# Kernel tuning notes

Hardware: AMD Instinct MI355X
Metric: run time of the kernel (lower is better)

## Reference

```python
import jax, jax.numpy as jnp
import numpy as np

HEAD_SIZE = 128
BLOCK_SIZE = 2048


def setup_inputs() -> dict:
    key = jax.random.key(0)
    kx, kk, kq, kv = jax.random.split(key, 4)
    B, T, C = 8, 2048, HEAD_SIZE
    s = 1.0 / np.sqrt(C)
    x = jax.random.normal(kx, (B, T, C), dtype=jnp.float32)
    Wk = jax.random.normal(kk, (C, C), dtype=jnp.float32) * s
    Wq = jax.random.normal(kq, (C, C), dtype=jnp.float32) * s
    Wv = jax.random.normal(kv, (C, C), dtype=jnp.float32) * s
    return {"x": x, "Wk": Wk, "Wq": Wq, "Wv": Wv}


def reference(x, Wk, Wq, Wv):
    B, T, C = x.shape
    # nn.Linear(C, C, bias=False): y = x @ W.T
    k = jnp.einsum('btc,dc->btd', x, Wk)
    q = jnp.einsum('btc,dc->btd', x, Wq)
    v = jnp.einsum('btc,dc->btd', x, Wv)
    scores = jnp.einsum('btd,bsd->bts', q, k) * (C ** -0.5)  # [B,T,T]
    causal = jnp.tril(jnp.ones((T, T), dtype=bool))
    scores = jnp.where(causal, scores, -jnp.inf)
    weights = jax.nn.softmax(scores, axis=-1)
    return jnp.einsum('bts,bsd->btd', weights, v)
```

## Files before the change

kernel.cpp:

```cpp
#include <hip/hip_runtime.h>

#define T_SEQ 2048
#define C_DIM 128
#define S_QK 0.08838834764831845f

typedef __attribute__((ext_vector_type(8))) short bf16x8;
typedef __attribute__((ext_vector_type(4))) float f32x4;

#define OPART_OFF 12582912UL
#define ML_OFF    31457280UL
#define XBF_OFF   31752192UL
#define WBF_OFF   35946496UL

__device__ __forceinline__ unsigned short f2bf(float f) {
    union { float f; unsigned int u; } v; v.f = f;
    unsigned int r = v.u + 0x7FFFu + ((v.u >> 16) & 1u);
    return (unsigned short)(r >> 16);
}

__device__ __forceinline__ int chunk_base(int qt) {
    int g = qt >> 3;
    if (g == 1) return (qt - 8) * 2;
    if (g == 2) return 16 + (qt - 16) * 3;
    return 40 + (qt - 24) * 4;
}

__global__ __launch_bounds__(256) void prep_kernel(
    const float* __restrict__ x,
    const float* __restrict__ Wk, const float* __restrict__ Wq,
    const float* __restrict__ Wv,
    unsigned short* __restrict__ xbf, unsigned short* __restrict__ wbf)
{
    int idx = blockIdx.x * 256 + threadIdx.x;
    const float* src;
    unsigned short* dst;
    float scale = 1.0f;
    if (idx < 524288) {
        src = x + (size_t)idx * 4;
        dst = xbf + (size_t)idx * 4;
    } else {
        int wi  = idx - 524288;
        int sel = wi >> 12;
        int off = (wi & 4095) * 4;
        src = (sel == 0 ? Wq : sel == 1 ? Wk : Wv) + off;
        dst = wbf + sel * 16384 + off;
        if (sel == 0) scale = S_QK;
    }
    float4 v = *reinterpret_cast<const float4*>(src);
    ushort4 o;
    o.x = f2bf(v.x * scale); o.y = f2bf(v.y * scale);
    o.z = f2bf(v.z * scale); o.w = f2bf(v.w * scale);
    *reinterpret_cast<ushort4*>(dst) = o;
}

__global__ __launch_bounds__(256) void proj_kernel(
    const unsigned short* __restrict__ xbf,
    const unsigned short* __restrict__ wbf,
    unsigned short* __restrict__ qo, unsigned short* __restrict__ ko,
    unsigned short* __restrict__ vto)
{
    const int rt = blockIdx.x;
    const int z  = blockIdx.y;
    const int tid  = threadIdx.x;
    const int lane = tid & 63;
    const int w    = tid >> 6;
    const int n16  = lane & 15;
    const int quad = lane >> 4;

    __shared__ __align__(16) unsigned short Wl[128 * 136];
    __shared__ __align__(16) unsigned short Xl[9216];

    const unsigned short* Wsrc = wbf + z * 16384;
    #pragma unroll
    for (int i = 0; i < 8; ++i) {
        int e = (tid + i * 256) * 8;
        int r = e >> 7, c = e & 127;
        *reinterpret_cast<uint4*>(&Wl[r * 136 + c]) =
            *reinterpret_cast<const uint4*>(Wsrc + e);
    }
    const unsigned short* xrow = xbf + (size_t)rt * 64 * C_DIM;
    #pragma unroll
    for (int i = 0; i < 4; ++i) {
        int e = (tid + i * 256) * 8;
        int r = e >> 7, c = e & 127;
        *reinterpret_cast<uint4*>(&Xl[r * 136 + c]) =
            *reinterpret_cast<const uint4*>(xrow + e);
    }
    __syncthreads();

    const int arow = w * 16 + n16;
    bf16x8 afr[4];
    #pragma unroll
    for (int kk = 0; kk < 4; ++kk)
        afr[kk] = *reinterpret_cast<const bf16x8*>(&Xl[arow * 136 + kk * 32 + quad * 8]);

    f32x4 acc[8];
    #pragma unroll
    for (int nt = 0; nt < 8; ++nt) acc[nt] = (f32x4){0.f, 0.f, 0.f, 0.f};
    #pragma unroll
    for (int kk = 0; kk < 4; ++kk)
        #pragma unroll
        for (int nt = 0; nt < 8; ++nt) {
            bf16x8 bfr = *reinterpret_cast<const bf16x8*>(
                &Wl[(nt * 16 + n16) * 136 + kk * 32 + quad * 8]);
            acc[nt] = __builtin_amdgcn_mfma_f32_16x16x32_bf16(afr[kk], bfr, acc[nt], 0, 0, 0);
        }

    const int trow_base = w * 16 + quad * 4;
    __syncthreads();
    if (z < 2) {
        #pragma unroll
        for (int nt = 0; nt < 8; ++nt)
            #pragma unroll
            for (int r = 0; r < 4; ++r)
                Xl[(trow_base + r) * 136 + nt * 16 + n16] = f2bf(acc[nt][r]);
        __syncthreads();
        unsigned short* dst = (z == 0 ? qo : ko) + (size_t)rt * 64 * C_DIM;
        #pragma unroll
        for (int i = 0; i < 4; ++i) {
            int e = (tid + i * 256) * 8;
            int r = e >> 7, c = e & 127;
            *reinterpret_cast<uint4*>(dst + e) =
                *reinterpret_cast<const uint4*>(&Xl[r * 136 + c]);
        }
    } else {
        const int b  = rt >> 5;
        const int qt = rt & 31;
        #pragma unroll
        for (int nt = 0; nt < 8; ++nt)
            #pragma unroll
            for (int r = 0; r < 4; ++r)
                Xl[(nt * 16 + n16) * 72 + trow_base + r] = f2bf(acc[nt][r]);
        __syncthreads();
        unsigned short* dst = vto + (size_t)b * C_DIM * T_SEQ + (size_t)qt * 64;
        #pragma unroll
        for (int i = 0; i < 4; ++i) {
            int e = tid + i * 256;
            int d = e >> 3, cv = (e & 7) * 8;
            *reinterpret_cast<uint4*>(dst + (size_t)d * T_SEQ + cv) =
                *reinterpret_cast<const uint4*>(&Xl[d * 72 + cv]);
        }
    }
}

__global__ __launch_bounds__(256) void attn_kernel(
    const unsigned short* __restrict__ qb,
    const unsigned short* __restrict__ kb,
    const unsigned short* __restrict__ vtb,
    float* __restrict__ opart, float2* __restrict__ mlbuf,
    float* __restrict__ out)
{
    const int qt    = blockIdx.x;
    const int chunk = blockIdx.y;
    const int b     = blockIdx.z;
    if (chunk * 8 > qt) return;

    const int tid  = threadIdx.x;
    const int lane = tid & 63;
    const int w    = tid >> 6;
    const int n16  = lane & 15;
    const int quad = lane >> 4;

    __shared__ __align__(16) unsigned short Kl[64 * 136];
    __shared__ __align__(16) unsigned short Vl[128 * 72];
    __shared__ __align__(16) unsigned short Pl[4][16 * 72];

    const size_t bT = (size_t)b * T_SEQ;
    const int qbase = qt * 64 + w * 16;

    bf16x8 qfr[4];
    #pragma unroll
    for (int kk = 0; kk < 4; ++kk)
        qfr[kk] = *reinterpret_cast<const bf16x8*>(
            qb + (bT + qbase + n16) * C_DIM + kk * 32 + quad * 8);

    f32x4 o[8];
    #pragma unroll
    for (int ct = 0; ct < 8; ++ct) o[ct] = (f32x4){0.f, 0.f, 0.f, 0.f};
    float m[4], l[4];
    #pragma unroll
    for (int r = 0; r < 4; ++r) { m[r] = -INFINITY; l[r] = 0.f; }

    const int k0 = chunk * 8;
    const int k1 = min(k0 + 8, qt + 1);

    for (int kt = k0; kt < k1; ++kt) {
        __syncthreads();
        const unsigned short* ks = kb + (bT + (size_t)kt * 64) * C_DIM;
        #pragma unroll
        for (int i = 0; i < 4; ++i) {
            int e = tid + i * 256;
            int r = e >> 4, c = (e & 15) * 8;
            *reinterpret_cast<uint4*>(&Kl[r * 136 + c]) =
                *reinterpret_cast<const uint4*>(ks + r * 128 + c);
        }
        const unsigned short* vs = vtb + (size_t)b * C_DIM * T_SEQ + (size_t)kt * 64;
        #pragma unroll
        for (int i = 0; i < 4; ++i) {
            int e = tid + i * 256;
            int d = e >> 3, c = (e & 7) * 8;
            *reinterpret_cast<uint4*>(&Vl[d * 72 + c]) =
                *reinterpret_cast<const uint4*>(vs + (size_t)d * T_SEQ + c);
        }
        __syncthreads();

        f32x4 s[4];
        #pragma unroll
        for (int nt = 0; nt < 4; ++nt) s[nt] = (f32x4){0.f, 0.f, 0.f, 0.f};
        #pragma unroll
        for (int kk = 0; kk < 4; ++kk)
            #pragma unroll
            for (int nt = 0; nt < 4; ++nt) {
                bf16x8 bfr = *reinterpret_cast<const bf16x8*>(
                    &Kl[(nt * 16 + n16) * 136 + kk * 32 + quad * 8]);
                s[nt] = __builtin_amdgcn_mfma_f32_16x16x32_bf16(qfr[kk], bfr, s[nt], 0, 0, 0);
            }

        if (kt == qt) {
            #pragma unroll
            for (int nt = 0; nt < 4; ++nt)
                #pragma unroll
                for (int r = 0; r < 4; ++r) {
                    int sabs = kt * 64 + nt * 16 + n16;
                    int qabs = qbase + quad * 4 + r;
                    if (sabs > qabs) s[nt][r] = -1e30f;
                }
        }

        float alpha[4];
        #pragma unroll
        for (int r = 0; r < 4; ++r) {
            float tmax = fmaxf(fmaxf(s[0][r], s[1][r]), fmaxf(s[2][r], s[3][r]));
            #pragma unroll
            for (int off = 1; off < 16; off <<= 1)
                tmax = fmaxf(tmax, __shfl_xor(tmax, off));
            float mn = fmaxf(m[r], tmax);
            alpha[r] = __expf(m[r] - mn);
            float tsum = 0.f;
            #pragma unroll
            for (int nt = 0; nt < 4; ++nt) {
                float p = __expf(s[nt][r] - mn);
                s[nt][r] = p;
                tsum += p;
            }
            #pragma unroll
            for (int off = 1; off < 16; off <<= 1)
                tsum += __shfl_xor(tsum, off);
            l[r] = l[r] * alpha[r] + tsum;
            m[r] = mn;
        }
        #pragma unroll
        for (int ct = 0; ct < 8; ++ct)
            #pragma unroll
            for (int r = 0; r < 4; ++r)
                o[ct][r] *= alpha[r];

        unsigned short* pw = Pl[w];
        #pragma unroll
        for (int nt = 0; nt < 4; ++nt)
            #pragma unroll
            for (int r = 0; r < 4; ++r)
                pw[(quad * 4 + r) * 72 + nt * 16 + n16] = f2bf(s[nt][r]);

        #pragma unroll
        for (int kk2 = 0; kk2 < 2; ++kk2) {
            bf16x8 afr = *reinterpret_cast<const bf16x8*>(
                &pw[n16 * 72 + kk2 * 32 + quad * 8]);
            #pragma unroll
            for (int ct = 0; ct < 8; ++ct) {
                bf16x8 bfr = *reinterpret_cast<const bf16x8*>(
                    &Vl[(ct * 16 + n16) * 72 + kk2 * 32 + quad * 8]);
                o[ct] = __builtin_amdgcn_mfma_f32_16x16x32_bf16(afr, bfr, o[ct], 0, 0, 0);
            }
        }
    }

    if (qt < 8) {
        float* outp = out + (bT + qbase) * C_DIM;
        #pragma unroll
        for (int r = 0; r < 4; ++r) {
            float inv = 1.0f / l[r];
            #pragma unroll
            for (int ct = 0; ct < 8; ++ct)
                outp[(size_t)(quad * 4 + r) * C_DIM + ct * 16 + n16] = o[ct][r] * inv;
        }
    } else {
        const int slot = b * 72 + chunk_base(qt) + chunk;
        float* op = opart + (size_t)slot * 8192;
        #pragma unroll
        for (int r = 0; r < 4; ++r) {
            int row = w * 16 + quad * 4 + r;
            #pragma unroll
            for (int ct = 0; ct < 8; ++ct)
                op[row * 128 + ct * 16 + n16] = o[ct][r];
            if (n16 == 0)
                mlbuf[(size_t)slot * 64 + row] = make_float2(m[r], l[r]);
        }
    }
}

__global__ __launch_bounds__(256) void merge_kernel(
    const float* __restrict__ opart, const float2* __restrict__ mlbuf,
    float* __restrict__ out)
{
    const int qt = 8 + blockIdx.x;
    const int b  = blockIdx.y;
    const int nch  = (qt >> 3) + 1;
    const int base = b * 72 + chunk_base(qt);
    const int row = threadIdx.x >> 2;
    const int c0  = (threadIdx.x & 3) * 32;

    float mi[4], li[4], wgt[4];
    float M = -INFINITY;
    for (int i = 0; i < nch; ++i) {
        float2 t = mlbuf[(size_t)(base + i) * 64 + row];
        mi[i] = t.x; li[i] = t.y;
        M = fmaxf(M, t.x);
    }
    float L = 0.f;
    for (int i = 0; i < nch; ++i) {
        wgt[i] = __expf(mi[i] - M);
        L += li[i] * wgt[i];
    }
    const float inv = 1.0f / L;

    float* orow = out + ((size_t)(b * T_SEQ + qt * 64 + row)) * C_DIM;
    #pragma unroll
    for (int j = 0; j < 8; ++j) {
        int col = c0 + j * 4;
        float ax = 0.f, ay = 0.f, az = 0.f, aw = 0.f;
        for (int i = 0; i < nch; ++i) {
            float4 p = *reinterpret_cast<const float4*>(
                opart + (size_t)(base + i) * 8192 + row * 128 + col);
            ax += wgt[i] * p.x; ay += wgt[i] * p.y;
            az += wgt[i] * p.z; aw += wgt[i] * p.w;
        }
        float4 r4; r4.x = ax * inv; r4.y = ay * inv; r4.z = az * inv; r4.w = aw * inv;
        *reinterpret_cast<float4*>(orow + col) = r4;
    }
}

extern "C" void kernel_launch(void* const* d_in, const int* in_sizes, int n_in,
                              void* d_out, int out_size, void* d_ws, size_t ws_size,
                              hipStream_t stream) {
    const float* x  = (const float*)d_in[0];
    const float* Wk = (const float*)d_in[1];
    const float* Wq = (const float*)d_in[2];
    const float* Wv = (const float*)d_in[3];

    unsigned short* qw  = (unsigned short*)d_ws;
    unsigned short* kw  = qw + 2097152;
    unsigned short* vw  = kw + 2097152;
    float*          opart = (float*)((char*)d_ws + OPART_OFF);
    float2*         mlb   = (float2*)((char*)d_ws + ML_OFF);
    unsigned short* xbf   = (unsigned short*)((char*)d_ws + XBF_OFF);
    unsigned short* wbf   = (unsigned short*)((char*)d_ws + WBF_OFF);

    prep_kernel<<<2096, 256, 0, stream>>>(x, Wk, Wq, Wv, xbf, wbf);
    proj_kernel<<<dim3(256, 3), 256, 0, stream>>>(xbf, wbf, qw, kw, vw);
    attn_kernel<<<dim3(32, 4, 8), 256, 0, stream>>>(qw, kw, vw, opart, mlb, (float*)d_out);
    merge_kernel<<<dim3(24, 8), 256, 0, stream>>>(opart, mlb, (float*)d_out);
}
```

Baseline: 135.7 us.

## Fuse bf16 conversion into projection, split KV finer, prefetch tiles, bf16 partials

Drops the separate prep kernel: the projection kernel now reads fp32 x and weights directly and converts them to bf16 while staging into shared memory. Attention KV chunks shrink from 8 to 4 tiles, which doubles the split-K grid to improve load balance, and the merge kernel now handles up to 8 partials. The next K/V tiles are prefetched into registers during compute. Partial outputs are stored as bf16 to halve merge traffic. The costs are extra partial slots, higher register pressure, and a small precision loss in the partials.

```diff
diff --git a/kernel.cpp b/kernel.cpp
--- a/kernel.cpp
+++ b/kernel.cpp
@@ -7,55 +7,27 @@
 typedef __attribute__((ext_vector_type(8))) short bf16x8;
 typedef __attribute__((ext_vector_type(4))) float f32x4;
 
-#define OPART_OFF 12582912UL
-#define ML_OFF    31457280UL
-#define XBF_OFF   31752192UL
-#define WBF_OFF   35946496UL
+#define ML_OFF 30932992UL
 
 __device__ __forceinline__ unsigned short f2bf(float f) {
     union { float f; unsigned int u; } v; v.f = f;
     unsigned int r = v.u + 0x7FFFu + ((v.u >> 16) & 1u);
     return (unsigned short)(r >> 16);
 }
-
-__device__ __forceinline__ int chunk_base(int qt) {
-    int g = qt >> 3;
-    if (g == 1) return (qt - 8) * 2;
-    if (g == 2) return 16 + (qt - 16) * 3;
-    return 40 + (qt - 24) * 4;
-}
-
-__global__ __launch_bounds__(256) void prep_kernel(
+__device__ __forceinline__ float bf2f(unsigned short s) {
+    union { unsigned int u; float f; } v; v.u = ((unsigned int)s) << 16;
+    return v.f;
+}
+
+__device__ __forceinline__ int chunk_base4(int qt) {
+    int g = qt >> 2;
+    return 2 * (g - 1) * (g + 2) + (qt - 4 * g) * (g + 1);
+}
+
+__global__ __launch_bounds__(256) void proj_kernel(
     const float* __restrict__ x,
-    const float* __restrict__ Wk, const float* __restrict__ Wq,
+    const float* __restrict__ Wq, const float* __restrict__ Wk,
     const float* __restrict__ Wv,
-    unsigned short* __restrict__ xbf, unsigned short* __restrict__ wbf)
-{
-    int idx = blockIdx.x * 256 + threadIdx.x;
-    const float* src;
-    unsigned short* dst;
-    float scale = 1.0f;
-    if (idx < 524288) {
-        src = x + (size_t)idx * 4;
-        dst = xbf + (size_t)idx * 4;
-    } else {
-        int wi  = idx - 524288;
-        int sel = wi >> 12;
-        int off = (wi & 4095) * 4;
-        src = (sel == 0 ? Wq : sel == 1 ? Wk : Wv) + off;
-        dst = wbf + sel * 16384 + off;
-        if (sel == 0) scale = S_QK;
-    }
-    float4 v = *reinterpret_cast<const float4*>(src);
-    ushort4 o;
-    o.x = f2bf(v.x * scale); o.y = f2bf(v.y * scale);
-    o.z = f2bf(v.z * scale); o.w = f2bf(v.w * scale);
-    *reinterpret_cast<ushort4*>(dst) = o;
-}
-
-__global__ __launch_bounds__(256) void proj_kernel(
-    const unsigned short* __restrict__ xbf,
-    const unsigned short* __restrict__ wbf,
     unsigned short* __restrict__ qo, unsigned short* __restrict__ ko,
     unsigned short* __restrict__ vto)
 {
@@ -70,21 +42,28 @@
     __shared__ __align__(16) unsigned short Wl[128 * 136];
     __shared__ __align__(16) unsigned short Xl[9216];
 
-    const unsigned short* Wsrc = wbf + z * 16384;
+    const float* W = (z == 0) ? Wq : (z == 1) ? Wk : Wv;
+    const float scale = (z == 0) ? S_QK : 1.0f;
+
+    #pragma unroll
+    for (int i = 0; i < 16; ++i) {
+        int e = (tid + i * 256) * 4;
+        int r = e >> 7, c = e & 127;
+        float4 v = *reinterpret_cast<const float4*>(W + e);
+        ushort4 o4;
+        o4.x = f2bf(v.x * scale); o4.y = f2bf(v.y * scale);
+        o4.z = f2bf(v.z * scale); o4.w = f2bf(v.w * scale);
+        *reinterpret_cast<ushort4*>(&Wl[r * 136 + c]) = o4;
+    }
+    const float* xr = x + (size_t)rt * 64 * C_DIM;
     #pragma unroll
     for (int i = 0; i < 8; ++i) {
-        int e = (tid + i * 256) * 8;
+        int e = (tid + i * 256) * 4;
         int r = e >> 7, c = e & 127;
-        *reinterpret_cast<uint4*>(&Wl[r * 136 + c]) =
-            *reinterpret_cast<const uint4*>(Wsrc + e);
-    }
-    const unsigned short* xrow = xbf + (size_t)rt * 64 * C_DIM;
-    #pragma unroll
-    for (int i = 0; i < 4; ++i) {
-        int e = (tid + i * 256) * 8;
-        int r = e >> 7, c = e & 127;
-        *reinterpret_cast<uint4*>(&Xl[r * 136 + c]) =
-            *reinterpret_cast<const uint4*>(xrow + e);
+        float4 v = *reinterpret_cast<const float4*>(xr + e);
+        ushort4 o4;
+        o4.x = f2bf(v.x); o4.y = f2bf(v.y); o4.z = f2bf(v.z); o4.w = f2bf(v.w);
+        *reinterpret_cast<ushort4*>(&Xl[r * 136 + c]) = o4;
     }
     __syncthreads();
 
@@ -147,13 +126,13 @@
     const unsigned short* __restrict__ qb,
     const unsigned short* __restrict__ kb,
     const unsigned short* __restrict__ vtb,
-    float* __restrict__ opart, float2* __restrict__ mlbuf,
+    unsigned short* __restrict__ opart, float2* __restrict__ mlbuf,
     float* __restrict__ out)
 {
     const int qt    = blockIdx.x;
     const int chunk = blockIdx.y;
     const int b     = blockIdx.z;
-    if (chunk * 8 > qt) return;
+    if (chunk * 4 > qt) return;
 
     const int tid  = threadIdx.x;
     const int lane = tid & 63;
@@ -181,28 +160,53 @@
     #pragma unroll
     for (int r = 0; r < 4; ++r) { m[r] = -INFINITY; l[r] = 0.f; }
 
-    const int k0 = chunk * 8;
-    const int k1 = min(k0 + 8, qt + 1);
+    const int k0 = chunk * 4;
+    const int k1 = min(k0 + 4, qt + 1);
+
+    uint4 kreg[4], vreg[4];
+    {
+        const unsigned short* ks = kb + (bT + (size_t)k0 * 64) * C_DIM;
+        #pragma unroll
+        for (int i = 0; i < 4; ++i) {
+            int e = tid + i * 256;
+            kreg[i] = *reinterpret_cast<const uint4*>(ks + (e >> 4) * 128 + (e & 15) * 8);
+        }
+        const unsigned short* vs = vtb + (size_t)b * C_DIM * T_SEQ + (size_t)k0 * 64;
+        #pragma unroll
+        for (int i = 0; i < 4; ++i) {
+            int e = tid + i * 256;
+            vreg[i] = *reinterpret_cast<const uint4*>(vs + (size_t)(e >> 3) * T_SEQ + (e & 7) * 8);
+        }
+    }
 
     for (int kt = k0; kt < k1; ++kt) {
         __syncthreads();
-        const unsigned short* ks = kb + (bT + (size_t)kt * 64) * C_DIM;
-        #pragma unroll
-        for (int i = 0; i < 4; ++i) {
-            int e = tid + i * 256;
-            int r = e >> 4, c = (e & 15) * 8;
-            *reinterpret_cast<uint4*>(&Kl[r * 136 + c]) =
-                *reinterpret_cast<const uint4*>(ks + r * 128 + c);
-        }
-        const unsigned short* vs = vtb + (size_t)b * C_DIM * T_SEQ + (size_t)kt * 64;
-        #pragma unroll
-        for (int i = 0; i < 4; ++i) {
-            int e = tid + i * 256;
-            int d = e >> 3, c = (e & 7) * 8;
-            *reinterpret_cast<uint4*>(&Vl[d * 72 + c]) =
-                *reinterpret_cast<const uint4*>(vs + (size_t)d * T_SEQ + c);
+        #pragma unroll
+        for (int i = 0; i < 4; ++i) {
+            int e = tid + i * 256;
+            *reinterpret_cast<uint4*>(&Kl[(e >> 4) * 136 + (e & 15) * 8]) = kreg[i];
+        }
+        #pragma unroll
+        for (int i = 0; i < 4; ++i) {
+            int e = tid + i * 256;
+            *reinterpret_cast<uint4*>(&Vl[(e >> 3) * 72 + (e & 7) * 8]) = vreg[i];
         }
         __syncthreads();
+
+        if (kt + 1 < k1) {
+            const unsigned short* ks = kb + (bT + (size_t)(kt + 1) * 64) * C_DIM;
+            #pragma unroll
+            for (int i = 0; i < 4; ++i) {
+                int e = tid + i * 256;
+                kreg[i] = *reinterpret_cast<const uint4*>(ks + (e >> 4) * 128 + (e & 15) * 8);
+            }
+            const unsigned short* vs = vtb + (size_t)b * C_DIM * T_SEQ + (size_t)(kt + 1) * 64;
+            #pragma unroll
+            for (int i = 0; i < 4; ++i) {
+                int e = tid + i * 256;
+                vreg[i] = *reinterpret_cast<const uint4*>(vs + (size_t)(e >> 3) * T_SEQ + (e & 7) * 8);
+            }
+        }
 
         f32x4 s[4];
         #pragma unroll
@@ -275,7 +279,7 @@
         }
     }
 
-    if (qt < 8) {
+    if (qt < 4) {
         float* outp = out + (bT + qbase) * C_DIM;
         #pragma unroll
         for (int r = 0; r < 4; ++r) {
@@ -285,14 +289,14 @@
                 outp[(size_t)(quad * 4 + r) * C_DIM + ct * 16 + n16] = o[ct][r] * inv;
         }
     } else {
-        const int slot = b * 72 + chunk_base(qt) + chunk;
-        float* op = opart + (size_t)slot * 8192;
+        const int slot = b * 140 + chunk_base4(qt) + chunk;
+        unsigned short* op = opart + (size_t)slot * 8192;
         #pragma unroll
         for (int r = 0; r < 4; ++r) {
             int row = w * 16 + quad * 4 + r;
             #pragma unroll
             for (int ct = 0; ct < 8; ++ct)
-                op[row * 128 + ct * 16 + n16] = o[ct][r];
+                op[row * 128 + ct * 16 + n16] = f2bf(o[ct][r]);
             if (n16 == 0)
                 mlbuf[(size_t)slot * 64 + row] = make_float2(m[r], l[r]);
         }
@@ -300,17 +304,17 @@
 }
 
 __global__ __launch_bounds__(256) void merge_kernel(
-    const float* __restrict__ opart, const float2* __restrict__ mlbuf,
+    const unsigned short* __restrict__ opart, const float2* __restrict__ mlbuf,
     float* __restrict__ out)
 {
-    const int qt = 8 + blockIdx.x;
+    const int qt = 4 + blockIdx.x;
     const int b  = blockIdx.y;
-    const int nch  = (qt >> 3) + 1;
-    const int base = b * 72 + chunk_base(qt);
+    const int nch  = (qt >> 2) + 1;
+    const int base = b * 140 + chunk_base4(qt);
     const int row = threadIdx.x >> 2;
     const int c0  = (threadIdx.x & 3) * 32;
 
-    float mi[4], li[4], wgt[4];
+    float mi[8], li[8], wgt[8];
     float M = -INFINITY;
     for (int i = 0; i < nch; ++i) {
         float2 t = mlbuf[(size_t)(base + i) * 64 + row];
@@ -324,19 +328,35 @@
     }
     const float inv = 1.0f / L;
 
-    float* orow = out + ((size_t)(b * T_SEQ + qt * 64 + row)) * C_DIM;
-    #pragma unroll
-    for (int j = 0; j < 8; ++j) {
-        int col = c0 + j * 4;
-        float ax = 0.f, ay = 0.f, az = 0.f, aw = 0.f;
-        for (int i = 0; i < nch; ++i) {
-            float4 p = *reinterpret_cast<const float4*>(
-                opart + (size_t)(base + i) * 8192 + row * 128 + col);
-            ax += wgt[i] * p.x; ay += wgt[i] * p.y;
-            az += wgt[i] * p.z; aw += wgt[i] * p.w;
-        }
-        float4 r4; r4.x = ax * inv; r4.y = ay * inv; r4.z = az * inv; r4.w = aw * inv;
-        *reinterpret_cast<float4*>(orow + col) = r4;
+    float acc[32];
+    #pragma unroll
+    for (int j = 0; j < 32; ++j) acc[j] = 0.f;
+    for (int i = 0; i < nch; ++i) {
+        const unsigned short* op = opart + (size_t)(base + i) * 8192 + row * 128 + c0;
+        const float wg = wgt[i];
+        #pragma unroll
+        for (int j4 = 0; j4 < 4; ++j4) {
+            uint4 u = *reinterpret_cast<const uint4*>(op + j4 * 8);
+            unsigned int vals[4] = {u.x, u.y, u.z, u.w};
+            #pragma unroll
+            for (int h = 0; h < 4; ++h) {
+                union { unsigned int u; float f; } lo, hi;
+                lo.u = (vals[h] & 0xFFFFu) << 16;
+                hi.u = vals[h] & 0xFFFF0000u;
+                acc[j4 * 8 + h * 2]     += wg * lo.f;
+                acc[j4 * 8 + h * 2 + 1] += wg * hi.f;
+            }
+        }
+    }
+    float* orow = out + ((size_t)(b * T_SEQ + qt * 64 + row)) * C_DIM + c0;
+    #pragma unroll
+    for (int j4 = 0; j4 < 8; ++j4) {
+        float4 r4;
+        r4.x = acc[j4 * 4]     * inv;
+        r4.y = acc[j4 * 4 + 1] * inv;
+        r4.z = acc[j4 * 4 + 2] * inv;
+        r4.w = acc[j4 * 4 + 3] * inv;
+        *reinterpret_cast<float4*>(orow + j4 * 4) = r4;
     }
 }
 
@@ -348,16 +368,13 @@
     const float* Wq = (const float*)d_in[2];
     const float* Wv = (const float*)d_in[3];
 
-    unsigned short* qw  = (unsigned short*)d_ws;
-    unsigned short* kw  = qw + 2097152;
-    unsigned short* vw  = kw + 2097152;
-    float*          opart = (float*)((char*)d_ws + OPART_OFF);
+    unsigned short* qw    = (unsigned short*)d_ws;
+    unsigned short* kw    = qw + 2097152;
+    unsigned short* vw    = kw + 2097152;
+    unsigned short* opart = vw + 2097152;
     float2*         mlb   = (float2*)((char*)d_ws + ML_OFF);
-    unsigned short* xbf   = (unsigned short*)((char*)d_ws + XBF_OFF);
-    unsigned short* wbf   = (unsigned short*)((char*)d_ws + WBF_OFF);
-
-    prep_kernel<<<2096, 256, 0, stream>>>(x, Wk, Wq, Wv, xbf, wbf);
-    proj_kernel<<<dim3(256, 3), 256, 0, stream>>>(xbf, wbf, qw, kw, vw);
-    attn_kernel<<<dim3(32, 4, 8), 256, 0, stream>>>(qw, kw, vw, opart, mlb, (float*)d_out);
-    merge_kernel<<<dim3(24, 8), 256, 0, stream>>>(opart, mlb, (float*)d_out);
-}
+
+    proj_kernel<<<dim3(256, 3), 256, 0, stream>>>(x, Wq, Wk, Wv, qw, kw, vw);
+    attn_kernel<<<dim3(32, 8, 8), 256, 0, stream>>>(qw, kw, vw, opart, mlb, (float*)d_out);
+    merge_kernel<<<dim3(28, 8), 256, 0, stream>>>(opart, mlb, (float*)d_out);
+}
```

Measured after the change: 164.6 us. 21.3% more time.
